# Optimization experiments

Hardware: AMD Instinct MI355X
Metric: run time of the kernel (lower is better)

The kernel has to match this reference:

```python
import jax, jax.numpy as jnp
import numpy as np
import math

B, QLEN, DMODEL, NHEAD, SKV = 16, 1, 2048, 32, 4096
HEAD_DIM = DMODEL // NHEAD  # 64


def setup_inputs() -> dict:
    key = jax.random.key(0)
    ks = jax.random.split(key, 12)
    x = jax.random.normal(ks[0], (B, QLEN, DMODEL), dtype=jnp.float32)
    last_pos = jax.random.randint(ks[1], (B,), 0, SKV, dtype=jnp.int64)
    # mask: attend to cache positions <= last_pos (broadcast over heads and q)
    mask = (jnp.arange(SKV)[None, :] <= last_pos[:, None]).reshape(B, 1, 1, SKV)
    s = 1.0 / math.sqrt(DMODEL)
    Wq = jax.random.normal(ks[2], (DMODEL, DMODEL), dtype=jnp.float32) * s
    bq = jax.random.normal(ks[3], (DMODEL,), dtype=jnp.float32) * 0.02
    Wk = jax.random.normal(ks[4], (DMODEL, DMODEL), dtype=jnp.float32) * s
    bk = jax.random.normal(ks[5], (DMODEL,), dtype=jnp.float32) * 0.02
    Wv = jax.random.normal(ks[6], (DMODEL, DMODEL), dtype=jnp.float32) * s
    bv = jax.random.normal(ks[7], (DMODEL,), dtype=jnp.float32) * 0.02
    Wo = jax.random.normal(ks[8], (DMODEL, DMODEL), dtype=jnp.float32) * s
    bo = jax.random.normal(ks[9], (DMODEL,), dtype=jnp.float32) * 0.02
    # prefilled KV cache (float32, as in the module)
    cache_k = jax.random.normal(ks[10], (B, NHEAD, SKV, HEAD_DIM), dtype=jnp.float32)
    cache_v = jax.random.normal(ks[11], (B, NHEAD, SKV, HEAD_DIM), dtype=jnp.float32)
    return {"x": x, "last_pos": last_pos, "mask": mask, "Wq": Wq, "bq": bq,
            "Wk": Wk, "bk": bk, "Wv": Wv, "bv": bv, "Wo": Wo, "bo": bo,
            "cache_k": cache_k, "cache_v": cache_v}


def reference(x, last_pos, mask, Wq, bq, Wk, bk, Wv, bv, Wo, bo, cache_k, cache_v):
    bsz, seq_len, _ = x.shape  # decode path: seq_len == 1
    # QKV projections -> [B, H, S, D]
    q = (x @ Wq + bq).reshape(bsz, seq_len, NHEAD, HEAD_DIM).transpose(0, 2, 1, 3)
    k = (x @ Wk + bk).reshape(bsz, seq_len, NHEAD, HEAD_DIM).transpose(0, 2, 1, 3)
    v = (x @ Wv + bv).reshape(bsz, seq_len, NHEAD, HEAD_DIM).transpose(0, 2, 1, 3)
    # KV-cache scatter update at last_pos (seq_len == 1 branch of the original)
    bidx = jnp.arange(bsz)
    updated_kcache = cache_k.at[bidx, :, last_pos, :].set(k[:, :, 0, :].astype(jnp.float32))
    updated_vcache = cache_v.at[bidx, :, last_pos, :].set(v[:, :, 0, :].astype(jnp.float32))
    kf = updated_kcache.astype(q.dtype)
    vf = updated_vcache.astype(q.dtype)
    # scores: [B, H, Q, SKV]
    scores = jnp.einsum("bhqd,bhkd->bhqk", q, kf) / math.sqrt(HEAD_DIM)
    scores = jnp.where(mask, scores, jnp.finfo(scores.dtype).min)
    probs = jax.nn.softmax(scores.astype(jnp.float32), axis=-1).astype(q.dtype)
    out = jnp.einsum("bhqk,bhkd->bhqd", probs, vf)
    out = out.transpose(0, 2, 1, 3).reshape(bsz, seq_len, -1)
    out = out @ Wo + bo
    return out, updated_kcache, updated_vcache
```

## Files before the change

### kernel.cpp

```cpp
#include <hip/hip_runtime.h>
#include <math.h>

#define BB 16
#define DMODEL 2048
#define NHEAD 32
#define SKV 4096
#define HDIM 64
#define BH (BB*NHEAD)

typedef float f4 __attribute__((ext_vector_type(4)));

__global__ __launch_bounds__(256) void gemm_part(
    const float* __restrict__ src,
    const float* __restrict__ Wa, const float* __restrict__ Wb,
    const float* __restrict__ Wc,
    float* __restrict__ pa, float* __restrict__ pb, float* __restrict__ pc,
    int rows) {
  const float* W = (blockIdx.z == 0) ? Wa : ((blockIdx.z == 1) ? Wb : Wc);
  float* part    = (blockIdx.z == 0) ? pa : ((blockIdx.z == 1) ? pb : pc);
  __shared__ float xs[16][64];
  int tid = threadIdx.x;
  int i0 = blockIdx.y * rows;
  int o  = blockIdx.x * 1024 + tid * 4;
  int nx = 16 * rows;
  for (int t = tid * 4; t < nx; t += 1024) {
    int b = t / rows, i = t - b * rows;
    *(f4*)&xs[b][i] = *(const f4*)&src[b * DMODEL + i0 + i];
  }
  __syncthreads();
  f4 acc[16];
#pragma unroll
  for (int b = 0; b < 16; ++b) acc[b] = (f4)0.f;
#pragma unroll 4
  for (int i = 0; i < rows; ++i) {
    f4 w = *(const f4*)&W[(size_t)(i0 + i) * DMODEL + o];
#pragma unroll
    for (int b = 0; b < 16; ++b) {
      float xv = xs[b][i];
      acc[b] += xv * w;
    }
  }
  float* p = part + (size_t)blockIdx.y * (16 * DMODEL) + o;
#pragma unroll
  for (int b = 0; b < 16; ++b) *(f4*)&p[b * DMODEL] = acc[b];
}

__global__ __launch_bounds__(256) void gemm_reduce(
    const float* __restrict__ pa, const float* __restrict__ pb,
    const float* __restrict__ pc,
    const float* __restrict__ ba, const float* __restrict__ bb,
    const float* __restrict__ bc,
    float* __restrict__ da, float* __restrict__ db, float* __restrict__ dc,
    int ntiles) {
  const float* p    = (blockIdx.y == 0) ? pa : ((blockIdx.y == 1) ? pb : pc);
  const float* bias = (blockIdx.y == 0) ? ba : ((blockIdx.y == 1) ? bb : bc);
  float* dst        = (blockIdx.y == 0) ? da : ((blockIdx.y == 1) ? db : dc);
  int idx = blockIdx.x * 256 + threadIdx.x;
  float s = bias[idx & (DMODEL - 1)];
#pragma unroll 8
  for (int t = 0; t < ntiles; ++t) s += p[(size_t)t * (16 * DMODEL) + idx];
  dst[idx] = s;
}

__global__ __launch_bounds__(256) void k_copy_scores(
    const float* __restrict__ cacheK, const float* __restrict__ knew,
    const float* __restrict__ qv, const int* __restrict__ last_pos,
    float* __restrict__ outK, float* __restrict__ scores) {
  int bh = blockIdx.x >> 4;
  int j0 = (blockIdx.x & 15) << 8;
  int b = bh >> 5;
  int lp = last_pos[b];
  int tid = threadIdx.x;
  int wave = tid >> 6, lane = tid & 63, q4 = lane >> 4, l16 = lane & 15;
  int rbase = wave * 4 + q4;
  const f4 qf = ((const f4*)(qv + bh * HDIM))[l16];
  const f4 kn = ((const f4*)(knew + bh * HDIM))[l16];
  size_t base = ((size_t)bh * SKV + j0 + rbase) * 16 + l16;
  const f4* K4 = (const f4*)cacheK + base;
  f4* O4 = (f4*)outK + base;
  float* s = scores + (size_t)bh * SKV;
#pragma unroll
  for (int t = 0; t < 16; ++t) {
    int j = j0 + rbase + t * 16;
    f4 kv = __builtin_nontemporal_load(&K4[t * 256]);
    if (j == lp) kv = kn;
    __builtin_nontemporal_store(kv, &O4[t * 256]);
    float p = qf.x * kv.x + qf.y * kv.y + qf.z * kv.z + qf.w * kv.w;
    p += __shfl_xor(p, 1);
    p += __shfl_xor(p, 2);
    p += __shfl_xor(p, 4);
    p += __shfl_xor(p, 8);
    if (l16 == 0 && j <= lp) s[j] = p * 0.125f;
  }
}

__global__ __launch_bounds__(256) void softmax_k(
    float* __restrict__ scores, const int* __restrict__ last_pos,
    float* __restrict__ attn) {
  int bh = blockIdx.x;
  int b = bh >> 5;
  int n = last_pos[b] + 1;
  float* s = scores + (size_t)bh * SKV;
  int tid = threadIdx.x;
  if (tid < HDIM) attn[bh * HDIM + tid] = 0.f;
  __shared__ float red[4], red2[4];
  float m = -1e30f;
  for (int j = tid; j < n; j += 256) m = fmaxf(m, s[j]);
#pragma unroll
  for (int o = 1; o < 64; o <<= 1) m = fmaxf(m, __shfl_xor(m, o));
  if ((tid & 63) == 0) red[tid >> 6] = m;
  __syncthreads();
  m = fmaxf(fmaxf(red[0], red[1]), fmaxf(red[2], red[3]));
  float sum = 0.f;
  for (int j = tid; j < n; j += 256) {
    float e = __expf(s[j] - m);
    s[j] = e;
    sum += e;
  }
#pragma unroll
  for (int o = 1; o < 64; o <<= 1) sum += __shfl_xor(sum, o);
  if ((tid & 63) == 0) red2[tid >> 6] = sum;
  __syncthreads();
  sum = red2[0] + red2[1] + red2[2] + red2[3];
  float inv = 1.f / sum;
  for (int j = tid; j < n; j += 256) s[j] *= inv;
}

__global__ __launch_bounds__(256) void v_copy_pv(
    const float* __restrict__ cacheV, const float* __restrict__ vnew,
    const float* __restrict__ probs, const int* __restrict__ last_pos,
    float* __restrict__ outV, float* __restrict__ attn) {
  __shared__ float part[4][64];
  int bh = blockIdx.x >> 4;
  int j0 = (blockIdx.x & 15) << 8;
  int b = bh >> 5;
  int lp = last_pos[b];
  int tid = threadIdx.x;
  int wave = tid >> 6, lane = tid & 63, q4 = lane >> 4, l16 = lane & 15;
  int rbase = wave * 4 + q4;
  const f4 vn = ((const f4*)(vnew + bh * HDIM))[l16];
  size_t base = ((size_t)bh * SKV + j0 + rbase) * 16 + l16;
  const f4* V4 = (const f4*)cacheV + base;
  f4* O4 = (f4*)outV + base;
  const float* pr = probs + (size_t)bh * SKV;
  f4 acc = (f4)0.f;
#pragma unroll
  for (int t = 0; t < 16; ++t) {
    int j = j0 + rbase + t * 16;
    f4 vv = __builtin_nontemporal_load(&V4[t * 256]);
    if (j == lp) vv = vn;
    __builtin_nontemporal_store(vv, &O4[t * 256]);
    if (j <= lp) {
      float p = pr[j];
      acc += p * vv;
    }
  }
  acc.x += __shfl_xor(acc.x, 16); acc.x += __shfl_xor(acc.x, 32);
  acc.y += __shfl_xor(acc.y, 16); acc.y += __shfl_xor(acc.y, 32);
  acc.z += __shfl_xor(acc.z, 16); acc.z += __shfl_xor(acc.z, 32);
  acc.w += __shfl_xor(acc.w, 16); acc.w += __shfl_xor(acc.w, 32);
  if (q4 == 0) ((f4*)part[wave])[l16] = acc;
  __syncthreads();
  if (tid < 64) {
    float v0 = part[0][tid] + part[1][tid] + part[2][tid] + part[3][tid];
    atomicAdd(&attn[bh * HDIM + tid], v0);
  }
}

extern "C" void kernel_launch(void* const* d_in, const int* in_sizes, int n_in,
                              void* d_out, int out_size, void* d_ws, size_t ws_size,
                              hipStream_t stream) {
  const float* x        = (const float*)d_in[0];
  const int*   last_pos = (const int*)d_in[1];
  const float* Wq = (const float*)d_in[3];
  const float* bq = (const float*)d_in[4];
  const float* Wk = (const float*)d_in[5];
  const float* bk = (const float*)d_in[6];
  const float* Wv = (const float*)d_in[7];
  const float* bv = (const float*)d_in[8];
  const float* Wo = (const float*)d_in[9];
  const float* bo = (const float*)d_in[10];
  const float* cacheK = (const float*)d_in[11];
  const float* cacheV = (const float*)d_in[12];

  float* out  = (float*)d_out;
  float* outK = out + (size_t)BB * DMODEL;
  float* outV = outK + (size_t)BH * SKV * HDIM;

  float* ws   = (float*)d_ws;
  float* q    = ws;
  float* k    = ws + 32768;
  float* v    = ws + 65536;
  float* attn = ws + 98304;
  float* big  = ws + 131072;
  float* scores = big;
  float* pq = big;
  float* pk = big + 1048576;
  float* pv = big + 2097152;
  float* po = big;

  gemm_part<<<dim3(2, 32, 3), 256, 0, stream>>>(x, Wq, Wk, Wv, pq, pk, pv, 64);
  gemm_reduce<<<dim3(128, 3), 256, 0, stream>>>(pq, pk, pv, bq, bk, bv, q, k, v, 32);
  k_copy_scores<<<8192, 256, 0, stream>>>(cacheK, k, q, last_pos, outK, scores);
  softmax_k<<<512, 256, 0, stream>>>(scores, last_pos, attn);
  v_copy_pv<<<8192, 256, 0, stream>>>(cacheV, v, scores, last_pos, outV, attn);
  gemm_part<<<dim3(2, 32, 1), 256, 0, stream>>>(attn, Wo, Wo, Wo, po, po, po, 64);
  gemm_reduce<<<dim3(128, 1), 256, 0, stream>>>(po, po, po, bo, bo, bo, out, out, out, 32);
}
```

Baseline: 458.1 us.

## Fuse softmax into score and PV kernels via per-block partial max/sum stats

Removes the standalone softmax kernel. The score kernel now computes a per-block max and exp-sum and writes them to a small stats buffer. The PV kernel merges the 16 partial stats per head and normalizes the probabilities on the fly into shared memory. Zeroing of the attention accumulator moves into the QKV reduce kernel, and the GEMM tile sizes become compile-time constants. This saves one launch and a read-write pass over the scores, at the cost of extra exp work and redundant stat merging in every PV block.

```diff
diff --git a/kernel.cpp b/kernel.cpp
--- a/kernel.cpp
+++ b/kernel.cpp
@@ -14,31 +14,27 @@
     const float* __restrict__ src,
     const float* __restrict__ Wa, const float* __restrict__ Wb,
     const float* __restrict__ Wc,
-    float* __restrict__ pa, float* __restrict__ pb, float* __restrict__ pc,
-    int rows) {
+    float* __restrict__ pa, float* __restrict__ pb, float* __restrict__ pc) {
   const float* W = (blockIdx.z == 0) ? Wa : ((blockIdx.z == 1) ? Wb : Wc);
   float* part    = (blockIdx.z == 0) ? pa : ((blockIdx.z == 1) ? pb : pc);
   __shared__ float xs[16][64];
   int tid = threadIdx.x;
-  int i0 = blockIdx.y * rows;
+  int i0 = blockIdx.y * 64;
   int o  = blockIdx.x * 1024 + tid * 4;
-  int nx = 16 * rows;
-  for (int t = tid * 4; t < nx; t += 1024) {
-    int b = t / rows, i = t - b * rows;
+  {
+    int t = tid * 4;
+    int b = t >> 6, i = t & 63;
     *(f4*)&xs[b][i] = *(const f4*)&src[b * DMODEL + i0 + i];
   }
   __syncthreads();
   f4 acc[16];
 #pragma unroll
   for (int b = 0; b < 16; ++b) acc[b] = (f4)0.f;
-#pragma unroll 4
-  for (int i = 0; i < rows; ++i) {
+#pragma unroll 8
+  for (int i = 0; i < 64; ++i) {
     f4 w = *(const f4*)&W[(size_t)(i0 + i) * DMODEL + o];
 #pragma unroll
-    for (int b = 0; b < 16; ++b) {
-      float xv = xs[b][i];
-      acc[b] += xv * w;
-    }
+    for (int b = 0; b < 16; ++b) acc[b] += xs[b][i] * w;
   }
   float* p = part + (size_t)blockIdx.y * (16 * DMODEL) + o;
 #pragma unroll
@@ -51,23 +47,26 @@
     const float* __restrict__ ba, const float* __restrict__ bb,
     const float* __restrict__ bc,
     float* __restrict__ da, float* __restrict__ db, float* __restrict__ dc,
-    int ntiles) {
+    float* __restrict__ zbuf) {
   const float* p    = (blockIdx.y == 0) ? pa : ((blockIdx.y == 1) ? pb : pc);
   const float* bias = (blockIdx.y == 0) ? ba : ((blockIdx.y == 1) ? bb : bc);
   float* dst        = (blockIdx.y == 0) ? da : ((blockIdx.y == 1) ? db : dc);
   int idx = blockIdx.x * 256 + threadIdx.x;
+  if (zbuf && blockIdx.y == 0) zbuf[idx] = 0.f;
   float s = bias[idx & (DMODEL - 1)];
 #pragma unroll 8
-  for (int t = 0; t < ntiles; ++t) s += p[(size_t)t * (16 * DMODEL) + idx];
+  for (int t = 0; t < 32; ++t) s += p[(size_t)t * (16 * DMODEL) + idx];
   dst[idx] = s;
 }
 
 __global__ __launch_bounds__(256) void k_copy_scores(
     const float* __restrict__ cacheK, const float* __restrict__ knew,
     const float* __restrict__ qv, const int* __restrict__ last_pos,
-    float* __restrict__ outK, float* __restrict__ scores) {
+    float* __restrict__ outK, float* __restrict__ scores,
+    float* __restrict__ pstat) {
   int bh = blockIdx.x >> 4;
-  int j0 = (blockIdx.x & 15) << 8;
+  int blk = blockIdx.x & 15;
+  int j0 = blk << 8;
   int b = bh >> 5;
   int lp = last_pos[b];
   int tid = threadIdx.x;
@@ -79,6 +78,7 @@
   const f4* K4 = (const f4*)cacheK + base;
   f4* O4 = (f4*)outK + base;
   float* s = scores + (size_t)bh * SKV;
+  float fv[16];
 #pragma unroll
   for (int t = 0; t < 16; ++t) {
     int j = j0 + rbase + t * 16;
@@ -90,59 +90,67 @@
     p += __shfl_xor(p, 2);
     p += __shfl_xor(p, 4);
     p += __shfl_xor(p, 8);
-    if (l16 == 0 && j <= lp) s[j] = p * 0.125f;
-  }
-}
-
-__global__ __launch_bounds__(256) void softmax_k(
-    float* __restrict__ scores, const int* __restrict__ last_pos,
-    float* __restrict__ attn) {
-  int bh = blockIdx.x;
-  int b = bh >> 5;
-  int n = last_pos[b] + 1;
-  float* s = scores + (size_t)bh * SKV;
-  int tid = threadIdx.x;
-  if (tid < HDIM) attn[bh * HDIM + tid] = 0.f;
-  __shared__ float red[4], red2[4];
-  float m = -1e30f;
-  for (int j = tid; j < n; j += 256) m = fmaxf(m, s[j]);
-#pragma unroll
-  for (int o = 1; o < 64; o <<= 1) m = fmaxf(m, __shfl_xor(m, o));
-  if ((tid & 63) == 0) red[tid >> 6] = m;
-  __syncthreads();
-  m = fmaxf(fmaxf(red[0], red[1]), fmaxf(red[2], red[3]));
-  float sum = 0.f;
-  for (int j = tid; j < n; j += 256) {
-    float e = __expf(s[j] - m);
-    s[j] = e;
-    sum += e;
-  }
-#pragma unroll
-  for (int o = 1; o < 64; o <<= 1) sum += __shfl_xor(sum, o);
-  if ((tid & 63) == 0) red2[tid >> 6] = sum;
-  __syncthreads();
-  sum = red2[0] + red2[1] + red2[2] + red2[3];
-  float inv = 1.f / sum;
-  for (int j = tid; j < n; j += 256) s[j] *= inv;
+    p *= 0.125f;
+    bool valid = (j <= lp);
+    if (l16 == 0 && valid) s[j] = p;
+    fv[t] = valid ? p : -1e30f;
+  }
+  float m = fv[0];
+#pragma unroll
+  for (int t = 1; t < 16; ++t) m = fmaxf(m, fv[t]);
+  m = fmaxf(m, __shfl_xor(m, 16));
+  m = fmaxf(m, __shfl_xor(m, 32));
+  float se = 0.f;
+#pragma unroll
+  for (int t = 0; t < 16; ++t) se += __expf(fv[t] - m);
+  se += __shfl_xor(se, 16);
+  se += __shfl_xor(se, 32);
+  __shared__ float lm[4], ls[4];
+  if (lane == 0) { lm[wave] = m; ls[wave] = se; }
+  __syncthreads();
+  if (tid == 0) {
+    float M = fmaxf(fmaxf(lm[0], lm[1]), fmaxf(lm[2], lm[3]));
+    float S = ls[0] * __expf(lm[0] - M) + ls[1] * __expf(lm[1] - M)
+            + ls[2] * __expf(lm[2] - M) + ls[3] * __expf(lm[3] - M);
+    pstat[(bh * 16 + blk) * 2 + 0] = M;
+    pstat[(bh * 16 + blk) * 2 + 1] = S;
+  }
 }
 
 __global__ __launch_bounds__(256) void v_copy_pv(
     const float* __restrict__ cacheV, const float* __restrict__ vnew,
-    const float* __restrict__ probs, const int* __restrict__ last_pos,
+    const float* __restrict__ scores, const float* __restrict__ pstat,
+    const int* __restrict__ last_pos,
     float* __restrict__ outV, float* __restrict__ attn) {
+  __shared__ float sm[16], ss[16], sp[256];
   __shared__ float part[4][64];
   int bh = blockIdx.x >> 4;
   int j0 = (blockIdx.x & 15) << 8;
   int b = bh >> 5;
   int lp = last_pos[b];
   int tid = threadIdx.x;
+  if (tid < 16) {
+    sm[tid] = pstat[(bh * 16 + tid) * 2 + 0];
+    ss[tid] = pstat[(bh * 16 + tid) * 2 + 1];
+  }
+  __syncthreads();
+  float M = sm[0];
+#pragma unroll
+  for (int i = 1; i < 16; ++i) M = fmaxf(M, sm[i]);
+  float S = 0.f;
+#pragma unroll
+  for (int i = 0; i < 16; ++i) S += ss[i] * __expf(sm[i] - M);
+  float inv = 1.f / S;
+  int jj = j0 + tid;
+  sp[tid] = (jj <= lp) ? __expf(scores[(size_t)bh * SKV + jj] - M) * inv : 0.f;
+  __syncthreads();
+
   int wave = tid >> 6, lane = tid & 63, q4 = lane >> 4, l16 = lane & 15;
   int rbase = wave * 4 + q4;
   const f4 vn = ((const f4*)(vnew + bh * HDIM))[l16];
   size_t base = ((size_t)bh * SKV + j0 + rbase) * 16 + l16;
   const f4* V4 = (const f4*)cacheV + base;
   f4* O4 = (f4*)outV + base;
-  const float* pr = probs + (size_t)bh * SKV;
   f4 acc = (f4)0.f;
 #pragma unroll
   for (int t = 0; t < 16; ++t) {
@@ -150,10 +158,7 @@
     f4 vv = __builtin_nontemporal_load(&V4[t * 256]);
     if (j == lp) vv = vn;
     __builtin_nontemporal_store(vv, &O4[t * 256]);
-    if (j <= lp) {
-      float p = pr[j];
-      acc += p * vv;
-    }
+    acc += sp[rbase + t * 16] * vv;
   }
   acc.x += __shfl_xor(acc.x, 16); acc.x += __shfl_xor(acc.x, 32);
   acc.y += __shfl_xor(acc.y, 16); acc.y += __shfl_xor(acc.y, 32);
@@ -187,23 +192,23 @@
   float* outK = out + (size_t)BB * DMODEL;
   float* outV = outK + (size_t)BH * SKV * HDIM;
 
-  float* ws   = (float*)d_ws;
-  float* q    = ws;
-  float* k    = ws + 32768;
-  float* v    = ws + 65536;
-  float* attn = ws + 98304;
-  float* big  = ws + 131072;
-  float* scores = big;
+  float* ws    = (float*)d_ws;
+  float* q     = ws;
+  float* k     = ws + 32768;
+  float* v     = ws + 65536;
+  float* attn  = ws + 98304;
+  float* pstat = ws + 131072;
+  float* big   = ws + 147456;
   float* pq = big;
   float* pk = big + 1048576;
   float* pv = big + 2097152;
+  float* scores = big;
   float* po = big;
 
-  gemm_part<<<dim3(2, 32, 3), 256, 0, stream>>>(x, Wq, Wk, Wv, pq, pk, pv, 64);
-  gemm_reduce<<<dim3(128, 3), 256, 0, stream>>>(pq, pk, pv, bq, bk, bv, q, k, v, 32);
-  k_copy_scores<<<8192, 256, 0, stream>>>(cacheK, k, q, last_pos, outK, scores);
-  softmax_k<<<512, 256, 0, stream>>>(scores, last_pos, attn);
-  v_copy_pv<<<8192, 256, 0, stream>>>(cacheV, v, scores, last_pos, outV, attn);
-  gemm_part<<<dim3(2, 32, 1), 256, 0, stream>>>(attn, Wo, Wo, Wo, po, po, po, 64);
-  gemm_reduce<<<dim3(128, 1), 256, 0, stream>>>(po, po, po, bo, bo, bo, out, out, out, 32);
-}
+  gemm_part<<<dim3(2, 32, 3), 256, 0, stream>>>(x, Wq, Wk, Wv, pq, pk, pv);
+  gemm_reduce<<<dim3(128, 3), 256, 0, stream>>>(pq, pk, pv, bq, bk, bv, q, k, v, attn);
+  k_copy_scores<<<8192, 256, 0, stream>>>(cacheK, k, q, last_pos, outK, scores, pstat);
+  v_copy_pv<<<8192, 256, 0, stream>>>(cacheV, v, scores, pstat, last_pos, outV, attn);
+  gemm_part<<<dim3(2, 32, 1), 256, 0, stream>>>(attn, Wo, Wo, Wo, po, po, po);
+  gemm_reduce<<<dim3(128, 1), 256, 0, stream>>>(po, po, po, bo, bo, bo, out, out, out, nullptr);
+}
```

Measured after the change: 445.8 us. 1.03x faster.
